# Kernel optimization log

Measured on AMD Instinct MI355X. Metric: run time of the kernel, lower is better.

The kernel has to match this reference:

```python
import jax, jax.numpy as jnp
import numpy as np

N, L, E, H = 4, 2048, 1024, 16
DK = E // H  # 64

def setup_inputs() -> dict:
    key = jax.random.key(0)
    ks = jax.random.split(key, 5)
    scale = 0.02
    return {
        "x": jax.random.normal(ks[0], (N, L, E), dtype=jnp.float32),
        "Wq": jax.random.normal(ks[1], (E, E), dtype=jnp.float32) * scale,
        "Wk": jax.random.normal(ks[2], (E, E), dtype=jnp.float32) * scale,
        "Wv": jax.random.normal(ks[3], (E, E), dtype=jnp.float32) * scale,
        "Wo": jax.random.normal(ks[4], (E, E), dtype=jnp.float32) * scale,
    }

def reference(x, Wq, Wk, Wv, Wo):
    n, l, _ = x.shape
    # nn.Linear(bias=False): y = x @ W.T
    q = x @ Wq.T  # (n, l, H*DK)
    k = x @ Wk.T
    v = x @ Wv.T
    # Faithful to torch .view: plain reshape (NOT transpose-based head split)
    q = q.reshape(n, H, l, DK)
    k = k.reshape(n, H, l, DK)
    v = v.reshape(n, H, l, DK)
    scores = jnp.einsum('nhqd,nhkd->nhqk', q, k) / jnp.sqrt(jnp.float32(DK))
    attn = jax.nn.softmax(scores, axis=-1)
    out = jnp.einsum('nhqk,nhkd->nhqd', attn, v).reshape(n, l, H * DK)
    return out @ Wo.T
```

## Files before the change

### kernel.cpp

```cpp
#include <hip/hip_runtime.h>


#define DEVI __device__ __forceinline__

typedef _Float16 half8 __attribute__((ext_vector_type(8)));
typedef _Float16 half4 __attribute__((ext_vector_type(4)));
typedef float f32x4 __attribute__((ext_vector_type(4)));

DEVI void gload_lds16(const void* g, void* l) {
    __builtin_amdgcn_global_load_lds(
        (const __attribute__((address_space(1))) void*)g,
        (__attribute__((address_space(3))) void*)l,
        16, 0, 0);
}

DEVI f32x4 zero4() { f32x4 z = {0.f, 0.f, 0.f, 0.f}; return z; }

#if __has_builtin(__builtin_amdgcn_exp2f)
DEVI float fast_exp2(float x) { return __builtin_amdgcn_exp2f(x); }
#else
DEVI float fast_exp2(float x) { return exp2f(x); }
#endif

#if __has_builtin(__builtin_amdgcn_mfma_f32_16x16x16f16)
DEVI f32x4 mfma16(half4 a, half4 b, f32x4 c) {
    return __builtin_amdgcn_mfma_f32_16x16x16f16(a, b, c, 0, 0, 0);
}
#else
DEVI f32x4 mfma16(half4 a, half4 b, f32x4 c) {
    asm volatile("v_mfma_f32_16x16x16_f16 %0, %1, %2, %0"
                 : "+v"(c) : "v"(a), "v"(b));
    return c;
}
#endif

DEVI half8 lds_read8_swz(const _Float16* base, int row, int colbyte) {
    const char* p = (const char*)base;
    const int off = (row * 128 + colbyte) ^ ((row & 7) << 4);
    return *(const half8*)(p + off);
}

__global__ __launch_bounds__(256) void f2h_kernel(const float* __restrict__ s,
                                                  _Float16* __restrict__ d) {
    const size_t i = (size_t)blockIdx.x * 256 + threadIdx.x;
    const float4 v = ((const float4*)s)[i];
    half4 h;
    h[0] = (_Float16)v.x; h[1] = (_Float16)v.y;
    h[2] = (_Float16)v.z; h[3] = (_Float16)v.w;
    ((half4*)d)[i] = h;
}

template<int MODE>
__global__ __launch_bounds__(512, 2) void gemm2(const _Float16* __restrict__ A,
                                                const _Float16* __restrict__ B,
                                                void* __restrict__ Cout,
                                                float qscale) {
    constexpr int CPX = (MODE == 0) ? 96 : 32;
    alignas(16) __shared__ _Float16 As[2][16384];
    alignas(16) __shared__ _Float16 Bs[2][8192];
    const int t = threadIdx.x;
    const int lane = t & 63;
    const int w = t >> 6;
    const int wm = w >> 1;
    const int wn = w & 1;
    const int r16 = lane & 15;
    const int q4 = lane >> 4;
    const int nid = (blockIdx.x & 7) * CPX + (blockIdx.x >> 3);
    const int bm = (nid & 31) * 256;
    const int bn = (nid >> 5) * 128;
    const int srow = t >> 3;
    const int scol = ((t & 7) ^ (srow & 7)) * 8;

    f32x4 acc[4][4];
    #pragma unroll
    for (int mi = 0; mi < 4; ++mi)
        #pragma unroll
        for (int ni = 0; ni < 4; ++ni)
            acc[mi][ni] = zero4();

    auto stage = [&](int b, int kt) {
        #pragma unroll
        for (int i = 0; i < 4; ++i)
            gload_lds16(A + (size_t)(bm + i * 64 + srow) * 1024 + kt + scol,
                        &As[b][i * 4096 + t * 8]);
        #pragma unroll
        for (int i = 0; i < 2; ++i)
            gload_lds16(B + (size_t)(bn + i * 64 + srow) * 1024 + kt + scol,
                        &Bs[b][i * 4096 + t * 8]);
    };

    stage(0, 0);
    for (int it = 0; it < 16; ++it) {
        const int cb = it & 1;
        if (it < 15) {
            stage(cb ^ 1, (it + 1) * 64);
            asm volatile("s_waitcnt vmcnt(6)" ::: "memory");
        } else {
            asm volatile("s_waitcnt vmcnt(0)" ::: "memory");
        }
        __builtin_amdgcn_sched_barrier(0);
        __builtin_amdgcn_s_barrier();
        __builtin_amdgcn_sched_barrier(0);
        __builtin_amdgcn_s_setprio(1);
        #pragma unroll
        for (int kk = 0; kk < 2; ++kk) {
            half8 a[4], bf[4];
            #pragma unroll
            for (int mi = 0; mi < 4; ++mi)
                a[mi] = lds_read8_swz(As[cb], wm * 64 + mi * 16 + r16, (kk * 32 + q4 * 8) * 2);
            #pragma unroll
            for (int ni = 0; ni < 4; ++ni)
                bf[ni] = lds_read8_swz(Bs[cb], wn * 64 + ni * 16 + r16, (kk * 32 + q4 * 8) * 2);
            #pragma unroll
            for (int mi = 0; mi < 4; ++mi)
                #pragma unroll
                for (int ni = 0; ni < 4; ++ni)
                    acc[mi][ni] = __builtin_amdgcn_mfma_f32_16x16x32_f16(a[mi], bf[ni], acc[mi][ni], 0, 0, 0);
        }
        __builtin_amdgcn_s_setprio(0);
        asm volatile("" ::: "memory");
        __builtin_amdgcn_s_barrier();
        __builtin_amdgcn_sched_barrier(0);
    }

    if (MODE == 0) {
        const int which = bn >> 10;
        const int cb2 = bn & 1023;
        const float alpha = (which == 0) ? qscale : 1.0f;
        _Float16* C = (_Float16*)Cout + (size_t)which * 8388608;
        #pragma unroll
        for (int mi = 0; mi < 4; ++mi) {
            const int row = bm + wm * 64 + mi * 16 + q4 * 4;
            #pragma unroll
            for (int ni = 0; ni < 4; ++ni) {
                const int col = cb2 + wn * 64 + ni * 16 + r16;
                #pragma unroll
                for (int i = 0; i < 4; ++i)
                    C[(size_t)(row + i) * 1024 + col] = (_Float16)(acc[mi][ni][i] * alpha);
            }
        }
    } else {
        float* C = (float*)Cout;
        #pragma unroll
        for (int mi = 0; mi < 4; ++mi) {
            const int row = bm + wm * 64 + mi * 16 + q4 * 4;
            #pragma unroll
            for (int ni = 0; ni < 4; ++ni) {
                const int col = bn + wn * 64 + ni * 16 + r16;
                #pragma unroll
                for (int i = 0; i < 4; ++i)
                    C[(size_t)(row + i) * 1024 + col] = acc[mi][ni][i];
            }
        }
    }
}

__global__ __launch_bounds__(256) void repack_v(const _Float16* __restrict__ V,
                                                _Float16* __restrict__ V4) {
    __shared__ unsigned short lds[64 * 65];
    const int t = threadIdx.x;
    const int kt = blockIdx.x;
    const size_t hb = (size_t)blockIdx.y * 131072;
    const int r = t >> 2;
    const int c0 = (t & 3) * 16;
    const unsigned short* Vi = (const unsigned short*)V;
    #pragma unroll
    for (int jj = 0; jj < 2; ++jj) {
        union { uint4 u; unsigned short s[8]; } tmp;
        tmp.u = *(const uint4*)&Vi[hb + (size_t)(kt * 64 + r) * 64 + c0 + jj * 8];
        #pragma unroll
        for (int e = 0; e < 8; ++e)
            lds[r * 65 + c0 + jj * 8 + e] = tmp.s[e];
    }
    __syncthreads();
    const size_t ob = hb + (size_t)kt * 4096;
    const unsigned short* ls = lds;
    #pragma unroll
    for (int h = 0; h < 2; ++h) {
        half8 v;
        #pragma unroll
        for (int e = 0; e < 8; ++e) {
            const int idx = t * 16 + h * 8 + e;
            const int a = idx >> 8;
            const int d = (idx >> 2) & 63;
            const int j = idx & 3;
            unsigned short u = ls[(4 * a + j) * 65 + d];
            v[e] = *(const _Float16*)&u;
        }
        *(half8*)&V4[ob + t * 16 + h * 8] = v;
    }
}

__global__ __launch_bounds__(256) void attn_kernel(const _Float16* __restrict__ Q,
                                                   const _Float16* __restrict__ K,
                                                   const _Float16* __restrict__ V4,
                                                   _Float16* __restrict__ O) {
    alignas(16) __shared__ _Float16 Ks[2][64 * 64];
    alignas(16) __shared__ _Float16 Vs[2][64 * 64];
    const int t = threadIdx.x;
    const int lane = t & 63;
    const int w = t >> 6;
    const int nid = (blockIdx.x & 7) * 128 + (blockIdx.x >> 3);
    const size_t hb = (size_t)(nid >> 4) * 131072;
    const int qt = nid & 15;
    const int r16 = lane & 15;
    const int q4 = lane >> 4;
    const int sr = t >> 3;
    const int sc = t & 7;

    half8 aq[2][2];
    const int q0 = qt * 128 + w * 32;
    #pragma unroll
    for (int mi = 0; mi < 2; ++mi)
        #pragma unroll
        for (int kk = 0; kk < 2; ++kk)
            aq[mi][kk] = *(const half8*)&Q[hb + (size_t)(q0 + mi * 16 + r16) * 64 + kk * 32 + q4 * 8];

    f32x4 o[4][2];
    float lsum[2] = {0.f, 0.f};
    #pragma unroll
    for (int ni = 0; ni < 4; ++ni)
        #pragma unroll
        for (int mi = 0; mi < 2; ++mi)
            o[ni][mi] = zero4();

    const int R0 = sr, R1 = 32 + sr;
    const int scs0 = (sc ^ (R0 & 7)) * 8;
    const int scs1 = (sc ^ (R1 & 7)) * 8;

    {
        gload_lds16(&K[hb + (size_t)R0 * 64 + scs0],  &Ks[0][t * 8]);
        gload_lds16(&K[hb + (size_t)R1 * 64 + scs1],  &Ks[0][2048 + t * 8]);
        gload_lds16(&V4[hb + t * 8],                  &Vs[0][t * 8]);
        gload_lds16(&V4[hb + 2048 + t * 8],           &Vs[0][2048 + t * 8]);
    }
    __syncthreads();

    int pb = 0;
    for (int kt = 0; kt < 32; ++kt) {
        if (kt + 1 < 32) {
            const size_t tb = hb + (size_t)(kt + 1) * 4096;
            gload_lds16(&K[tb + (size_t)R0 * 64 + scs0],  &Ks[pb ^ 1][t * 8]);
            gload_lds16(&K[tb + (size_t)R1 * 64 + scs1],  &Ks[pb ^ 1][2048 + t * 8]);
            gload_lds16(&V4[tb + t * 8],                  &Vs[pb ^ 1][t * 8]);
            gload_lds16(&V4[tb + 2048 + t * 8],           &Vs[pb ^ 1][2048 + t * 8]);
        }

        f32x4 sT[4][2];
        #pragma unroll
        for (int ki = 0; ki < 4; ++ki)
            #pragma unroll
            for (int mi = 0; mi < 2; ++mi)
                sT[ki][mi] = zero4();
        __builtin_amdgcn_s_setprio(1);
        #pragma unroll
        for (int kk = 0; kk < 2; ++kk) {
            half8 ak[4];
            #pragma unroll
            for (int ki = 0; ki < 4; ++ki)
                ak[ki] = lds_read8_swz(Ks[pb], ki * 16 + r16, (kk * 32 + q4 * 8) * 2);
            #pragma unroll
            for (int ki = 0; ki < 4; ++ki)
                #pragma unroll
                for (int mi = 0; mi < 2; ++mi)
                    sT[ki][mi] = __builtin_amdgcn_mfma_f32_16x16x32_f16(ak[ki], aq[mi][kk], sT[ki][mi], 0, 0, 0);
        }
        __builtin_amdgcn_s_setprio(0);

        half4 pT[4][2];
        #pragma unroll
        for (int ki = 0; ki < 4; ++ki)
            #pragma unroll
            for (int mi = 0; mi < 2; ++mi) {
                const float p0 = fast_exp2(sT[ki][mi][0]);
                const float p1 = fast_exp2(sT[ki][mi][1]);
                const float p2 = fast_exp2(sT[ki][mi][2]);
                const float p3 = fast_exp2(sT[ki][mi][3]);
                lsum[mi] += (p0 + p1) + (p2 + p3);
                half4 pv;
                pv[0] = (_Float16)p0; pv[1] = (_Float16)p1;
                pv[2] = (_Float16)p2; pv[3] = (_Float16)p3;
                pT[ki][mi] = pv;
            }

        __builtin_amdgcn_s_setprio(1);
        #pragma unroll
        for (int ki = 0; ki < 4; ++ki)
            #pragma unroll
            for (int ni = 0; ni < 4; ++ni) {
                const half4 av = *(const half4*)&Vs[pb][(ki * 4 + q4) * 256 + (ni * 16 + r16) * 4];
                #pragma unroll
                for (int mi = 0; mi < 2; ++mi)
                    o[ni][mi] = mfma16(av, pT[ki][mi], o[ni][mi]);
            }
        __builtin_amdgcn_s_setprio(0);

        __syncthreads();
        pb ^= 1;
    }

    float inv[2];
    #pragma unroll
    for (int mi = 0; mi < 2; ++mi) {
        float l = lsum[mi];
        l += __shfl_xor(l, 16);
        l += __shfl_xor(l, 32);
        inv[mi] = 1.f / l;
    }
    #pragma unroll
    for (int mi = 0; mi < 2; ++mi) {
        const int q = q0 + mi * 16 + r16;
        #pragma unroll
        for (int ni = 0; ni < 4; ++ni) {
            half4 ov;
            #pragma unroll
            for (int i = 0; i < 4; ++i)
                ov[i] = (_Float16)(o[ni][mi][i] * inv[mi]);
            *(half4*)&O[hb + (size_t)q * 64 + ni * 16 + q4 * 4] = ov;
        }
    }
}

extern "C" void kernel_launch(void* const* d_in, const int* in_sizes, int n_in,
                              void* d_out, int out_size, void* d_ws, size_t ws_size,
                              hipStream_t stream) {
    const float* x  = (const float*)d_in[0];
    const float* Wq = (const float*)d_in[1];
    const float* Wk = (const float*)d_in[2];
    const float* Wv = (const float*)d_in[3];
    const float* Wo = (const float*)d_in[4];

    const size_t XSZ = (size_t)8192 * 1024;
    const size_t WSZ = (size_t)1024 * 1024;

    _Float16* ws  = (_Float16*)d_ws;
    _Float16* xh  = ws;
    _Float16* wqh = ws + XSZ;
    _Float16* wkh = wqh + WSZ;
    _Float16* wvh = wkh + WSZ;
    _Float16* woh = wvh + WSZ;
    _Float16* qh  = woh + WSZ;
    _Float16* kh  = qh + XSZ;
    _Float16* vh  = kh + XSZ;
    _Float16* aoh = vh + XSZ;
    _Float16* v4h = xh;

    f2h_kernel<<<XSZ / 4 / 256, 256, 0, stream>>>(x,  xh);
    f2h_kernel<<<WSZ / 4 / 256, 256, 0, stream>>>(Wq, wqh);
    f2h_kernel<<<WSZ / 4 / 256, 256, 0, stream>>>(Wk, wkh);
    f2h_kernel<<<WSZ / 4 / 256, 256, 0, stream>>>(Wv, wvh);
    f2h_kernel<<<WSZ / 4 / 256, 256, 0, stream>>>(Wo, woh);

    const float qscale = 0.125f * 1.44269504088896340736f;

    gemm2<0><<<768, 512, 0, stream>>>(xh, wqh, (void*)qh, qscale);

    repack_v<<<dim3(32, 64), 256, 0, stream>>>(vh, v4h);

    attn_kernel<<<1024, 256, 0, stream>>>(qh, kh, v4h, aoh);

    gemm2<1><<<256, 512, 0, stream>>>(aoh, woh, d_out, 1.0f);
    (void)in_sizes; (void)n_in; (void)out_size; (void)ws_size;
}
```

Baseline: 317.6 us.

## Replace double-buffered 256x128 GEMM with single-buffered 128x128 tiles and vector stores

Replaces the 512-thread, 256x128-tile, double-buffered GEMM with a 256-thread kernel that uses 128x128 tiles and a single LDS buffer guarded by __syncthreads, launching twice as many blocks. It also swaps the MFMA operand order so each lane holds four consecutive output columns, which allows half4 and float4 vector stores in the epilogue. The goal is more blocks for better occupancy and wider, coalesced output writes. In exchange it loses the overlap of global loads with compute and the priority and scheduling hints, so load latency is exposed on every k step.

```diff
diff --git a/kernel.cpp b/kernel.cpp
--- a/kernel.cpp
+++ b/kernel.cpp
@@ -51,25 +51,26 @@
 }
 
 template<int MODE>
-__global__ __launch_bounds__(512, 2) void gemm2(const _Float16* __restrict__ A,
-                                                const _Float16* __restrict__ B,
-                                                void* __restrict__ Cout,
-                                                float qscale) {
-    constexpr int CPX = (MODE == 0) ? 96 : 32;
-    alignas(16) __shared__ _Float16 As[2][16384];
-    alignas(16) __shared__ _Float16 Bs[2][8192];
+__global__ __launch_bounds__(256) void gemm_k(const _Float16* __restrict__ A,
+                                              const _Float16* __restrict__ B,
+                                              void* __restrict__ Cout,
+                                              float qscale) {
+    constexpr int NBLK = (MODE == 0) ? 24 : 8;
+    constexpr int CPX  = (MODE == 0) ? 192 : 64;
+    alignas(16) __shared__ _Float16 As[128 * 64];
+    alignas(16) __shared__ _Float16 Bs[128 * 64];
     const int t = threadIdx.x;
     const int lane = t & 63;
     const int w = t >> 6;
-    const int wm = w >> 1;
-    const int wn = w & 1;
+    const int wr = (w >> 1) * 64;
+    const int wc = (w & 1) * 64;
+    const int nid = (blockIdx.x & 7) * CPX + (blockIdx.x >> 3);
+    const int bn = (nid % NBLK) * 128;
+    const int bm = (nid / NBLK) * 128;
     const int r16 = lane & 15;
     const int q4 = lane >> 4;
-    const int nid = (blockIdx.x & 7) * CPX + (blockIdx.x >> 3);
-    const int bm = (nid & 31) * 256;
-    const int bn = (nid >> 5) * 128;
-    const int srow = t >> 3;
-    const int scol = ((t & 7) ^ (srow & 7)) * 8;
+    const int sr = t >> 3;
+    const int sc8 = ((t & 7) ^ (sr & 7)) * 8;
 
     f32x4 acc[4][4];
     #pragma unroll
@@ -78,51 +79,30 @@
         for (int ni = 0; ni < 4; ++ni)
             acc[mi][ni] = zero4();
 
-    auto stage = [&](int b, int kt) {
-        #pragma unroll
-        for (int i = 0; i < 4; ++i)
-            gload_lds16(A + (size_t)(bm + i * 64 + srow) * 1024 + kt + scol,
-                        &As[b][i * 4096 + t * 8]);
-        #pragma unroll
-        for (int i = 0; i < 2; ++i)
-            gload_lds16(B + (size_t)(bn + i * 64 + srow) * 1024 + kt + scol,
-                        &Bs[b][i * 4096 + t * 8]);
-    };
-
-    stage(0, 0);
-    for (int it = 0; it < 16; ++it) {
-        const int cb = it & 1;
-        if (it < 15) {
-            stage(cb ^ 1, (it + 1) * 64);
-            asm volatile("s_waitcnt vmcnt(6)" ::: "memory");
-        } else {
-            asm volatile("s_waitcnt vmcnt(0)" ::: "memory");
-        }
-        __builtin_amdgcn_sched_barrier(0);
-        __builtin_amdgcn_s_barrier();
-        __builtin_amdgcn_sched_barrier(0);
-        __builtin_amdgcn_s_setprio(1);
+    for (int kt = 0; kt < 1024; kt += 64) {
+        #pragma unroll
+        for (int i = 0; i < 4; ++i) {
+            gload_lds16(A + (size_t)(bm + i * 32 + sr) * 1024 + kt + sc8, &As[i * 2048 + t * 8]);
+            gload_lds16(B + (size_t)(bn + i * 32 + sr) * 1024 + kt + sc8, &Bs[i * 2048 + t * 8]);
+        }
+        __syncthreads();
         #pragma unroll
         for (int kk = 0; kk < 2; ++kk) {
-            half8 a[4], bf[4];
+            half8 a[4], b[4];
             #pragma unroll
             for (int mi = 0; mi < 4; ++mi)
-                a[mi] = lds_read8_swz(As[cb], wm * 64 + mi * 16 + r16, (kk * 32 + q4 * 8) * 2);
+                a[mi] = lds_read8_swz(As, wr + mi * 16 + r16, (kk * 32 + q4 * 8) * 2);
             #pragma unroll
             for (int ni = 0; ni < 4; ++ni)
-                bf[ni] = lds_read8_swz(Bs[cb], wn * 64 + ni * 16 + r16, (kk * 32 + q4 * 8) * 2);
+                b[ni] = lds_read8_swz(Bs, wc + ni * 16 + r16, (kk * 32 + q4 * 8) * 2);
             #pragma unroll
             for (int mi = 0; mi < 4; ++mi)
                 #pragma unroll
                 for (int ni = 0; ni < 4; ++ni)
-                    acc[mi][ni] = __builtin_amdgcn_mfma_f32_16x16x32_f16(a[mi], bf[ni], acc[mi][ni], 0, 0, 0);
-        }
-        __builtin_amdgcn_s_setprio(0);
-        asm volatile("" ::: "memory");
-        __builtin_amdgcn_s_barrier();
-        __builtin_amdgcn_sched_barrier(0);
-    }
-
+                    acc[mi][ni] = __builtin_amdgcn_mfma_f32_16x16x32_f16(b[ni], a[mi], acc[mi][ni], 0, 0, 0);
+        }
+        __syncthreads();
+    }
     if (MODE == 0) {
         const int which = bn >> 10;
         const int cb2 = bn & 1023;
@@ -130,26 +110,26 @@
         _Float16* C = (_Float16*)Cout + (size_t)which * 8388608;
         #pragma unroll
         for (int mi = 0; mi < 4; ++mi) {
-            const int row = bm + wm * 64 + mi * 16 + q4 * 4;
+            const int row = bm + wr + mi * 16 + r16;
             #pragma unroll
             for (int ni = 0; ni < 4; ++ni) {
-                const int col = cb2 + wn * 64 + ni * 16 + r16;
+                const int col0 = cb2 + wc + ni * 16 + q4 * 4;
+                half4 ov;
                 #pragma unroll
                 for (int i = 0; i < 4; ++i)
-                    C[(size_t)(row + i) * 1024 + col] = (_Float16)(acc[mi][ni][i] * alpha);
+                    ov[i] = (_Float16)(acc[mi][ni][i] * alpha);
+                *(half4*)&C[(size_t)row * 1024 + col0] = ov;
             }
         }
     } else {
         float* C = (float*)Cout;
         #pragma unroll
         for (int mi = 0; mi < 4; ++mi) {
-            const int row = bm + wm * 64 + mi * 16 + q4 * 4;
+            const int row = bm + wr + mi * 16 + r16;
             #pragma unroll
             for (int ni = 0; ni < 4; ++ni) {
-                const int col = bn + wn * 64 + ni * 16 + r16;
-                #pragma unroll
-                for (int i = 0; i < 4; ++i)
-                    C[(size_t)(row + i) * 1024 + col] = acc[mi][ni][i];
+                const int col0 = bn + wc + ni * 16 + q4 * 4;
+                *(f32x4*)&C[(size_t)row * 1024 + col0] = acc[mi][ni];
             }
         }
     }
@@ -353,12 +333,12 @@
 
     const float qscale = 0.125f * 1.44269504088896340736f;
 
-    gemm2<0><<<768, 512, 0, stream>>>(xh, wqh, (void*)qh, qscale);
+    gemm_k<0><<<1536, 256, 0, stream>>>(xh, wqh, (void*)qh, qscale);
 
     repack_v<<<dim3(32, 64), 256, 0, stream>>>(vh, v4h);
 
     attn_kernel<<<1024, 256, 0, stream>>>(qh, kh, v4h, aoh);
 
-    gemm2<1><<<256, 512, 0, stream>>>(aoh, woh, d_out, 1.0f);
+    gemm_k<1><<<512, 256, 0, stream>>>(aoh, woh, d_out, 1.0f);
     (void)in_sizes; (void)n_in; (void)out_size; (void)ws_size;
 }
```

Measured after the change: 318.9 us. About the same (+0.4%).
